# Optimization experiments

Measured on AMD Instinct MI355X. Metric: run time of the kernel, lower is better.

Reference implementation:

```python
import jax, jax.numpy as jnp
import numpy as np

B, C, H, Wd = 4096, 32, 14, 14
ENC_DIM = 512
ATT_DIM = 128


def setup_inputs() -> dict:
    key = jax.random.key(0)
    ks = jax.random.split(key, 10)
    s = 0.05
    return {
        "img_features": jax.random.normal(ks[0], (B, C, H, Wd), jnp.float32),
        "prev_hidden": jax.random.normal(ks[1], (B, ENC_DIM), jnp.float32),
        "W_w": jax.random.normal(ks[2], (ATT_DIM, C), jnp.float32) * s,
        "W_b": jnp.zeros((ATT_DIM,), jnp.float32),
        "U_w": jax.random.normal(ks[3], (ATT_DIM, ENC_DIM), jnp.float32) * s,
        "U_b": jnp.zeros((ATT_DIM,), jnp.float32),
        "v_w": jax.random.normal(ks[4], (1, ATT_DIM), jnp.float32) * s,
        "v_b": jnp.zeros((1,), jnp.float32),
        "fb_w": jax.random.normal(ks[5], (C, ENC_DIM), jnp.float32) * s,
        "fb_b": jnp.zeros((C,), jnp.float32),
    }


def reference(img_features, prev_hidden, W_w, W_b, U_w, U_b, v_w, v_b, fb_w, fb_b):
    b = img_features.shape[0]
    c = img_features.shape[1]
    # [B, C, H, W] -> [B, P, C] where P = H*W (spatial positions)
    img_parts = img_features.reshape(b, c, -1).transpose(0, 2, 1)
    W_s = jnp.einsum('bpc,ac->bpa', img_parts, W_w) + W_b          # [B, P, 128]
    U_h = prev_hidden @ U_w.T + U_b                                 # [B, 128]
    att = jnp.tanh(W_s + U_h[:, None, :])                           # [B, P, 128]
    score = jnp.einsum('bpa,a->bp', att, v_w[0]) + v_b[0]           # [B, P]
    att_weights = jax.nn.softmax(score, axis=1)                     # softmax over spatial
    context = jnp.einsum('bpc,bp->bc', img_parts, att_weights)      # [B, 32]
    beta = jax.nn.sigmoid(prev_hidden @ fb_w.T + fb_b)              # [B, 32]
    context = context * beta
    return (context, att_weights)
```

## Files before the change

kernel.cpp:

```cpp
#include <hip/hip_runtime.h>
#include <hip/hip_bf16.h>


typedef __attribute__((ext_vector_type(8))) short short8;
typedef __attribute__((ext_vector_type(8))) __bf16 bf16x8;
typedef __attribute__((ext_vector_type(4))) float floatx4;
typedef __attribute__((ext_vector_type(4))) unsigned int uint4v;

#define K2E 2.8853900817779268f

#if __has_builtin(__builtin_amdgcn_exp2f)
#define EXP2F(x) __builtin_amdgcn_exp2f(x)
#else
#define EXP2F(x) __expf(0.6931471805599453f * (x))
#endif

static __device__ __forceinline__ float bf2f(unsigned short u) {
    union { unsigned int i; float f; } v; v.i = ((unsigned int)u) << 16; return v.f;
}
static __device__ __forceinline__ unsigned short f2bf(float f) {
    union { float f; unsigned int i; } v; v.f = f;
    unsigned int r = v.i + 0x7FFFu + ((v.i >> 16) & 1u);
    return (unsigned short)(r >> 16);
}
static __device__ __forceinline__ float sigmoid_rcp(float x) {
    return __builtin_amdgcn_rcpf(1.0f + __expf(-x));
}
static __device__ __forceinline__ void split_trunc8(const float* src, bf16x8* hi, bf16x8* lo) {
    uint4v u0 = *(const uint4v*)src;
    uint4v u1 = *(const uint4v*)(src + 4);
    unsigned int fb[8], lb[8];
#pragma unroll
    for (int j = 0; j < 4; j++) { fb[j] = u0[j]; fb[4 + j] = u1[j]; }
#pragma unroll
    for (int k = 0; k < 8; k++) {
        float x = __uint_as_float(fb[k]);
        float h = __uint_as_float(fb[k] & 0xFFFF0000u);
        lb[k] = __float_as_uint(x - h);
    }
    uint4v hp, lp;
#pragma unroll
    for (int j = 0; j < 4; j++) {
        hp[j] = __builtin_amdgcn_perm(fb[2 * j + 1], fb[2 * j], 0x07060302u);
        lp[j] = __builtin_amdgcn_perm(lb[2 * j + 1], lb[2 * j], 0x07060302u);
    }
    *hi = __builtin_bit_cast(bf16x8, hp);
    *lo = __builtin_bit_cast(bf16x8, lp);
}

__global__ __launch_bounds__(256) void k0_split(
    const float* __restrict__ U_w, const float* __restrict__ fb_w,
    const float* __restrict__ W_w,
    unsigned short* __restrict__ Bhi, unsigned short* __restrict__ Blo,
    unsigned short* __restrict__ Whi)
{
    int i = blockIdx.x * 256 + threadIdx.x;
    if (i < 81920) {
        float x = (i < 65536) ? U_w[i] : fb_w[i - 65536];
        unsigned short h = f2bf(x);
        Bhi[i] = h;
        Blo[i] = f2bf(x - bf2f(h));
    } else {
        Whi[i - 81920] = f2bf(W_w[i - 81920] * K2E);
    }
}

__global__ __launch_bounds__(256) void k1_gemm(
    const float* __restrict__ hidden,
    const unsigned short* __restrict__ Bhi, const unsigned short* __restrict__ Blo,
    const float* __restrict__ U_b, const float* __restrict__ W_b,
    const float* __restrict__ fb_b,
    float* __restrict__ uh_out, float* __restrict__ beta_out,
    float* __restrict__ partial, int nsplit, int direct)
{
    const int tid = threadIdx.x;
    const int wave = tid >> 6, lane = tid & 63, quad = lane >> 4, l16 = lane & 15;
    const int mgroup = blockIdx.x / nsplit;
    const int s = blockIdx.x % nsplit;
    const int mtile = mgroup * 4 + wave;
    const int kblock = 512 / nsplit;
    const int ks0 = s * kblock;
    const int ksteps = kblock >> 5;
    const int arow = mtile * 16 + l16;

    floatx4 acc[10];
#pragma unroll
    for (int i = 0; i < 10; i++) acc[i] = (floatx4)(0.0f);

    for (int ksi = 0; ksi < ksteps; ksi++) {
        const int e0 = ks0 + ksi * 32 + quad * 8;
        bf16x8 ah, al;
        split_trunc8(hidden + (size_t)arow * 512 + e0, &ah, &al);
#pragma unroll
        for (int n = 0; n < 10; n++) {
            const size_t bo = (size_t)(n * 16 + l16) * 512 + e0;
            bf16x8 bh = *(const bf16x8*)(Bhi + bo);
            bf16x8 bl = *(const bf16x8*)(Blo + bo);
            acc[n] = __builtin_amdgcn_mfma_f32_16x16x32_bf16(ah, bl, acc[n], 0, 0, 0);
            acc[n] = __builtin_amdgcn_mfma_f32_16x16x32_bf16(al, bh, acc[n], 0, 0, 0);
            acc[n] = __builtin_amdgcn_mfma_f32_16x16x32_bf16(ah, bh, acc[n], 0, 0, 0);
        }
    }

#pragma unroll
    for (int n = 0; n < 10; n++) {
        const int col = n * 16 + l16;
#pragma unroll
        for (int r = 0; r < 4; r++) {
            if (direct) {
                const int m = mtile * 16 + quad * 4 + r;
                if (col < 128)
                    uh_out[(size_t)m * 128 + col] = K2E * (acc[n][r] + U_b[col] + W_b[col]);
                else
                    beta_out[(size_t)m * 32 + (col - 128)] =
                        sigmoid_rcp(acc[n][r] + fb_b[col - 128]);
            } else {
                partial[(size_t)(mtile * nsplit + s) * 2560 + (quad * 4 + r) * 160 + col]
                    = acc[n][r];
            }
        }
    }
}

__global__ __launch_bounds__(256) void k1b_reduce(
    const float* __restrict__ partial,
    const float* __restrict__ U_b, const float* __restrict__ W_b,
    const float* __restrict__ fb_b,
    float* __restrict__ uh_out, float* __restrict__ beta_out, int nsplit)
{
    const int idx = blockIdx.x * 256 + threadIdx.x;
    const int mt = idx / 2560, r = idx % 2560;
    float v = 0.0f;
    for (int s = 0; s < nsplit; s++)
        v += partial[(size_t)(mt * nsplit + s) * 2560 + r];
    const int m = mt * 16 + r / 160, col = r % 160;
    if (col < 128) uh_out[(size_t)m * 128 + col] = K2E * (v + U_b[col] + W_b[col]);
    else beta_out[(size_t)m * 32 + (col - 128)] = sigmoid_rcp(v + fb_b[col - 128]);
}

#define HSTR 40

__global__ __launch_bounds__(256, 4) void k2_attn(
    const float* __restrict__ img,
    const unsigned short* __restrict__ Whi,
    const float* __restrict__ v_w,
    const float* __restrict__ uh,
    const float* __restrict__ beta,
    float* __restrict__ out)
{
    __shared__ __align__(16) unsigned short s_imgh[208 * HSTR];
    __shared__ float s_score[208];
    __shared__ float s_red[4];
    __shared__ float s_ctx[4][32];

    const int tid = threadIdx.x;
    const int b = blockIdx.x;
    const int wave = tid >> 6, lane = tid & 63, quad = lane >> 4, l16 = lane & 15;

    if (tid < 196) {
        const float* src = img + (size_t)b * 6272 + tid;
#pragma unroll
        for (int h = 0; h < 2; h++) {
            float v[16];
#pragma unroll
            for (int j = 0; j < 16; j++) v[j] = src[(size_t)(h * 16 + j) * 196];
            unsigned int hb[16];
#pragma unroll
            for (int j = 0; j < 16; j++) {
                unsigned int u = __float_as_uint(v[j]);
                hb[j] = u + 0x7FFFu + ((u >> 16) & 1u);
            }
            uint4v hp0, hp1;
#pragma unroll
            for (int j = 0; j < 4; j++) {
                hp0[j] = __builtin_amdgcn_perm(hb[2 * j + 1], hb[2 * j], 0x07060302u);
                hp1[j] = __builtin_amdgcn_perm(hb[8 + 2 * j + 1], hb[8 + 2 * j], 0x07060302u);
            }
            *(uint4v*)&s_imgh[tid * HSTR + h * 16] = hp0;
            *(uint4v*)&s_imgh[tid * HSTR + h * 16 + 8] = hp1;
        }
    } else {
        for (int i = tid - 196; i < 12 * HSTR; i += 60) s_imgh[196 * HSTR + i] = 0;
        if (tid < 208) s_score[tid] = 0.0f;
    }

    float uaR[8], va2R[8], sv = 0.0f;
#pragma unroll
    for (int nt = 0; nt < 8; nt++) {
        uaR[nt] = uh[(size_t)b * 128 + nt * 16 + l16];
        float v = v_w[nt * 16 + l16];
        sv += v;
        va2R[nt] = -2.0f * v;
    }
    sv += __shfl_xor(sv, 1); sv += __shfl_xor(sv, 2);
    sv += __shfl_xor(sv, 4); sv += __shfl_xor(sv, 8);
    __syncthreads();

    float esum = 0.0f;
    for (int mt = wave; mt < 13; mt += 4) {
        bf16x8 a = *(const bf16x8*)&s_imgh[(mt * 16 + l16) * HSTR + quad * 8];
        float sc4[4] = {0.f, 0.f, 0.f, 0.f};
#pragma unroll
        for (int nt = 0; nt < 8; nt++) {
            bf16x8 bh = *(const bf16x8*)(Whi + (nt * 16 + l16) * 32 + quad * 8);
            const float ua = uaR[nt];
            floatx4 d = {ua, ua, ua, ua};
            d = __builtin_amdgcn_mfma_f32_16x16x32_bf16(a, bh, d, 0, 0, 0);
#pragma unroll
            for (int r = 0; r < 4; r++) {
                float e = EXP2F(d[r]);
                float rr = __builtin_amdgcn_rcpf(1.0f + e);
                sc4[r] = __builtin_fmaf(va2R[nt], rr, sc4[r]);
            }
        }
#pragma unroll
        for (int r = 0; r < 4; r++) {
            float s = sc4[r];
            s += __shfl_xor(s, 1); s += __shfl_xor(s, 2);
            s += __shfl_xor(s, 4); s += __shfl_xor(s, 8);
            const int p = mt * 16 + quad * 4 + r;
            if (l16 == 0 && p < 196) {
                float e = __expf(sv + s);
                s_score[p] = e;
                esum += e;
            }
        }
    }
    esum += __shfl_xor(esum, 16);
    esum += __shfl_xor(esum, 32);
    if (lane == 0) s_red[wave] = esum;
    __syncthreads();

    const float tot = s_red[0] + s_red[1] + s_red[2] + s_red[3];
    const float rtot = __builtin_amdgcn_rcpf(tot);
    if (tid < 196)
        out[131072 + (size_t)b * 196 + tid] = s_score[tid] * rtot;

    {
        const int c2 = (lane & 15) * 2;
        const int po = wave * 4 + (lane >> 4);
        float a0 = 0.0f, a1 = 0.0f;
#pragma unroll
        for (int j = 0; j < 13; j++) {
            const int p = po + j * 16;
            const unsigned int pair = *(const unsigned int*)&s_imgh[p * HSTR + c2];
            const float w = s_score[p];
            a0 = __builtin_fmaf(bf2f((unsigned short)(pair & 0xFFFFu)), w, a0);
            a1 = __builtin_fmaf(bf2f((unsigned short)(pair >> 16)), w, a1);
        }
        a0 += __shfl_xor(a0, 16); a0 += __shfl_xor(a0, 32);
        a1 += __shfl_xor(a1, 16); a1 += __shfl_xor(a1, 32);
        if (lane < 16) {
            s_ctx[wave][c2] = a0;
            s_ctx[wave][c2 + 1] = a1;
        }
    }
    __syncthreads();
    if (tid < 32) {
        const float v = s_ctx[0][tid] + s_ctx[1][tid] + s_ctx[2][tid] + s_ctx[3][tid];
        out[(size_t)b * 32 + tid] = v * rtot * beta[(size_t)b * 32 + tid];
    }
}

extern "C" void kernel_launch(void* const* d_in, const int* in_sizes, int n_in,
                              void* d_out, int out_size, void* d_ws, size_t ws_size,
                              hipStream_t stream) {
    const float* img    = (const float*)d_in[0];
    const float* hidden = (const float*)d_in[1];
    const float* W_w    = (const float*)d_in[2];
    const float* W_b    = (const float*)d_in[3];
    const float* U_w    = (const float*)d_in[4];
    const float* U_b    = (const float*)d_in[5];
    const float* v_w    = (const float*)d_in[6];
    const float* fb_w   = (const float*)d_in[8];
    const float* fb_b   = (const float*)d_in[9];
    float* out = (float*)d_out;

    float* uh_ws   = (float*)d_ws;
    float* beta_ws = uh_ws + 4096 * 128;
    unsigned short* Bhi = (unsigned short*)(beta_ws + 4096 * 32);
    unsigned short* Blo = Bhi + 81920;
    unsigned short* Whi = Blo + 81920;
    float* partial = (float*)(Whi + 4096);
    const size_t fixed_bytes = ((char*)partial) - ((char*)d_ws);

    int nsplit = 1, direct = 1;
    if (ws_size >= fixed_bytes + (size_t)256 * 4 * 2560 * 4) { nsplit = 4; direct = 0; }
    else if (ws_size >= fixed_bytes + (size_t)256 * 2 * 2560 * 4) { nsplit = 2; direct = 0; }
    else if (ws_size >= fixed_bytes + (size_t)256 * 1 * 2560 * 4) { nsplit = 1; direct = 0; }

    k0_split<<<dim3(336), dim3(256), 0, stream>>>(U_w, fb_w, W_w, Bhi, Blo, Whi);
    k1_gemm<<<dim3(64 * nsplit), dim3(256), 0, stream>>>(
        hidden, Bhi, Blo, U_b, W_b, fb_b, uh_ws, beta_ws, partial, nsplit, direct);
    if (!direct)
        k1b_reduce<<<dim3(2560), dim3(256), 0, stream>>>(
            partial, U_b, W_b, fb_b, uh_ws, beta_ws, nsplit);
    k2_attn<<<dim3(4096), dim3(256), 0, stream>>>(img, Whi, v_w, uh_ws, beta_ws, out);
}
```

Before: 207.7 us.

## Load image directly into MFMA registers, stage W in LDS, raise split count

```diff
diff --git a/kernel.cpp b/kernel.cpp
--- a/kernel.cpp
+++ b/kernel.cpp
@@ -138,8 +138,6 @@
     else beta_out[(size_t)m * 32 + (col - 128)] = sigmoid_rcp(v + fb_b[col - 128]);
 }
 
-#define HSTR 40
-
 __global__ __launch_bounds__(256, 4) void k2_attn(
     const float* __restrict__ img,
     const unsigned short* __restrict__ Whi,
@@ -148,7 +146,7 @@
     const float* __restrict__ beta,
     float* __restrict__ out)
 {
-    __shared__ __align__(16) unsigned short s_imgh[208 * HSTR];
+    __shared__ __align__(16) unsigned short s_w[4096];
     __shared__ float s_score[208];
     __shared__ float s_red[4];
     __shared__ float s_ctx[4][32];
@@ -156,33 +154,17 @@
     const int tid = threadIdx.x;
     const int b = blockIdx.x;
     const int wave = tid >> 6, lane = tid & 63, quad = lane >> 4, l16 = lane & 15;
-
-    if (tid < 196) {
-        const float* src = img + (size_t)b * 6272 + tid;
-#pragma unroll
-        for (int h = 0; h < 2; h++) {
-            float v[16];
-#pragma unroll
-            for (int j = 0; j < 16; j++) v[j] = src[(size_t)(h * 16 + j) * 196];
-            unsigned int hb[16];
-#pragma unroll
-            for (int j = 0; j < 16; j++) {
-                unsigned int u = __float_as_uint(v[j]);
-                hb[j] = u + 0x7FFFu + ((u >> 16) & 1u);
-            }
-            uint4v hp0, hp1;
-#pragma unroll
-            for (int j = 0; j < 4; j++) {
-                hp0[j] = __builtin_amdgcn_perm(hb[2 * j + 1], hb[2 * j], 0x07060302u);
-                hp1[j] = __builtin_amdgcn_perm(hb[8 + 2 * j + 1], hb[8 + 2 * j], 0x07060302u);
-            }
-            *(uint4v*)&s_imgh[tid * HSTR + h * 16] = hp0;
-            *(uint4v*)&s_imgh[tid * HSTR + h * 16 + 8] = hp1;
-        }
-    } else {
-        for (int i = tid - 196; i < 12 * HSTR; i += 60) s_imgh[196 * HSTR + i] = 0;
-        if (tid < 208) s_score[tid] = 0.0f;
-    }
+    const float* imgb = img + (size_t)b * 6272;
+
+    if (tid < 128) {
+        const int nt = tid >> 4, al = tid & 15;
+#pragma unroll
+        for (int q = 0; q < 4; q++) {
+            uint4v w = *(const uint4v*)(Whi + tid * 32 + q * 8);
+            *(uint4v*)&s_w[((nt * 4 + q) * 16 + al) * 8] = w;
+        }
+    }
+    if (tid >= 196 && tid < 208) s_score[tid] = 0.0f;
 
     float uaR[8], va2R[8], sv = 0.0f;
 #pragma unroll
@@ -198,11 +180,24 @@
 
     float esum = 0.0f;
     for (int mt = wave; mt < 13; mt += 4) {
-        bf16x8 a = *(const bf16x8*)&s_imgh[(mt * 16 + l16) * HSTR + quad * 8];
+        const int p = mt * 16 + l16;
+        const int pl = (p < 196) ? p : 195;
+        unsigned int hb[8];
+#pragma unroll
+        for (int j = 0; j < 8; j++) {
+            unsigned int u = __float_as_uint(imgb[(quad * 8 + j) * 196 + pl]);
+            hb[j] = u + 0x7FFFu + ((u >> 16) & 1u);
+        }
+        uint4v hp;
+#pragma unroll
+        for (int j = 0; j < 4; j++)
+            hp[j] = __builtin_amdgcn_perm(hb[2 * j + 1], hb[2 * j], 0x07060302u);
+        bf16x8 a = __builtin_bit_cast(bf16x8, hp);
+
         float sc4[4] = {0.f, 0.f, 0.f, 0.f};
 #pragma unroll
         for (int nt = 0; nt < 8; nt++) {
-            bf16x8 bh = *(const bf16x8*)(Whi + (nt * 16 + l16) * 32 + quad * 8);
+            bf16x8 bh = *(const bf16x8*)&s_w[((nt * 4 + quad) * 16 + l16) * 8];
             const float ua = uaR[nt];
             floatx4 d = {ua, ua, ua, ua};
             d = __builtin_amdgcn_mfma_f32_16x16x32_bf16(a, bh, d, 0, 0, 0);
@@ -218,10 +213,10 @@
             float s = sc4[r];
             s += __shfl_xor(s, 1); s += __shfl_xor(s, 2);
             s += __shfl_xor(s, 4); s += __shfl_xor(s, 8);
-            const int p = mt * 16 + quad * 4 + r;
-            if (l16 == 0 && p < 196) {
+            const int pr = mt * 16 + quad * 4 + r;
+            if (l16 == 0 && pr < 196) {
                 float e = __expf(sv + s);
-                s_score[p] = e;
+                s_score[pr] = e;
                 esum += e;
             }
         }
@@ -243,10 +238,10 @@
 #pragma unroll
         for (int j = 0; j < 13; j++) {
             const int p = po + j * 16;
-            const unsigned int pair = *(const unsigned int*)&s_imgh[p * HSTR + c2];
+            const int pl = (p < 196) ? p : 195;
             const float w = s_score[p];
-            a0 = __builtin_fmaf(bf2f((unsigned short)(pair & 0xFFFFu)), w, a0);
-            a1 = __builtin_fmaf(bf2f((unsigned short)(pair >> 16)), w, a1);
+            a0 = __builtin_fmaf(imgb[c2 * 196 + pl], w, a0);
+            a1 = __builtin_fmaf(imgb[(c2 + 1) * 196 + pl], w, a1);
         }
         a0 += __shfl_xor(a0, 16); a0 += __shfl_xor(a0, 32);
         a1 += __shfl_xor(a1, 16); a1 += __shfl_xor(a1, 32);
@@ -285,9 +280,9 @@
     const size_t fixed_bytes = ((char*)partial) - ((char*)d_ws);
 
     int nsplit = 1, direct = 1;
-    if (ws_size >= fixed_bytes + (size_t)256 * 4 * 2560 * 4) { nsplit = 4; direct = 0; }
+    if (ws_size >= fixed_bytes + (size_t)256 * 8 * 2560 * 4) { nsplit = 8; direct = 0; }
+    else if (ws_size >= fixed_bytes + (size_t)256 * 4 * 2560 * 4) { nsplit = 4; direct = 0; }
     else if (ws_size >= fixed_bytes + (size_t)256 * 2 * 2560 * 4) { nsplit = 2; direct = 0; }
-    else if (ws_size >= fixed_bytes + (size_t)256 * 1 * 2560 * 4) { nsplit = 1; direct = 0; }
 
     k0_split<<<dim3(336), dim3(256), 0, stream>>>(U_w, fb_w, W_w, Bhi, Blo, Whi);
     k1_gemm<<<dim3(64 * nsplit), dim3(256), 0, stream>>>(
```

Measured after the change: 247.0 us. 1.19x slower.
